# Kernel tuning notes

Measured on AMD Instinct MI355X. Metric: run time of the kernel, lower is better.

Reference implementation:

```python
import jax, jax.numpy as jnp
import numpy as np
from jax import lax


def _causal_depthwise_conv(x, conv_w, conv_b):
    # x: [B, L, D]; conv_w: [D, 1, K]; conv_b: [D]
    K = conv_w.shape[-1]
    xc = jnp.transpose(x, (0, 2, 1))                      # [B, D, L]
    xc = jnp.pad(xc, ((0, 0), (0, 0), (K - 1, 0)))        # left (causal) pad
    D = xc.shape[1]
    y = lax.conv_general_dilated(
        xc, conv_w, window_strides=(1,), padding='VALID',
        dimension_numbers=('NCH', 'OIH', 'NCH'), feature_group_count=D)
    y = y + conv_b[None, :, None]
    return jnp.transpose(y, (0, 2, 1))                    # [B, L, D]


def setup_inputs() -> dict:
    key = jax.random.key(0)
    ks = jax.random.split(key, 7)
    B, L, Dm, S, K = 4, 4096, 2048, 512, 4
    s = 0.02
    x = jax.random.normal(ks[0], (B, L, Dm), dtype=jnp.float32)
    Wxproj = jax.random.normal(ks[1], (2 * S + 1, Dm), dtype=jnp.float32) * s
    Winproj = jax.random.normal(ks[2], (S, Dm), dtype=jnp.float32) * s
    Woutproj = jax.random.normal(ks[3], (Dm, S), dtype=jnp.float32) * s
    conv_w = jax.random.normal(ks[4], (Dm, 1, K), dtype=jnp.float32) * 0.5
    conv_b = jax.random.normal(ks[5], (Dm,), dtype=jnp.float32) * 0.02
    A_log = jnp.log(jnp.arange(1, S + 1, dtype=jnp.float32))
    D = jnp.ones((Dm,), dtype=jnp.float32)
    return {"x": x, "Wxproj": Wxproj, "Winproj": Winproj, "Woutproj": Woutproj,
            "conv_w": conv_w, "conv_b": conv_b, "A_log": A_log, "D": D}


def reference(x, Wxproj, Winproj, Woutproj, conv_w, conv_b, A_log, D):
    S = A_log.shape[0]
    # causal depthwise conv (Conv1d with padding=K-1, truncated to seq_len)
    x_conv = _causal_depthwise_conv(x, conv_w, conv_b)     # [B, L, Dm]
    # SSM parameters from raw x (matches original: x_proj applied to x, not x_conv)
    ssm_params = jnp.einsum('bld,pd->blp', x, Wxproj)      # [B, L, 2S+1]
    Bmat = ssm_params[..., :S]
    Cmat = ssm_params[..., S:2 * S]
    delta = jax.nn.softplus(ssm_params[..., 2 * S:])       # [B, L, 1]
    A = -jnp.exp(A_log)                                    # [S]
    deltaA = jnp.exp(A[None, None, :] * delta)             # [B, L, S]
    x_state = jnp.einsum('bld,sd->bls', x_conv, Winproj)   # [B, L, S]
    Bu = delta * Bmat * x_state                            # [B, L, S]
    # h_t = deltaA_t * h_{t-1} + Bu_t  via associative scan
    def combine(c1, c2):
        a1, b1 = c1
        a2, b2 = c2
        return a1 * a2, a2 * b1 + b2
    _, h = lax.associative_scan(combine, (deltaA, Bu), axis=1)  # [B, L, S]
    h_mod = Cmat * h
    out = jnp.einsum('bls,ds->bld', h_mod, Woutproj) + D[None, None, :] * x_conv
    return out
```

## Files before the change

kernel.cpp:

```cpp
#include <hip/hip_runtime.h>
#include <math.h>

typedef __bf16 bf16_t;
typedef __bf16 bf16x8 __attribute__((ext_vector_type(8)));
typedef __bf16 bf16x4 __attribute__((ext_vector_type(4)));
typedef float  f32x4  __attribute__((ext_vector_type(4)));

constexpr int Bb  = 4;
constexpr int L   = 4096;
constexpr int Dm  = 2048;
constexpr int S   = 512;
constexpr int M   = Bb * L;
constexpr int NP  = 2 * S + 1;
constexpr int NP_PAD = 1280;
constexpr int CL  = 128;
constexpr int NCH = L / CL;
constexpr int TL  = 32;
constexpr int NTC = L / TL;

#define AS1 __attribute__((address_space(1)))
#define AS3 __attribute__((address_space(3)))

__global__ __launch_bounds__(256)
void f2b_kernel(const float* __restrict__ in, bf16_t* __restrict__ out,
                long out8, long in_elems)
{
    long i = (long)blockIdx.x * 256 + threadIdx.x;
    if (i >= out8) return;
    long e = i * 8;
    bf16x8 o;
    if (e + 8 <= in_elems) {
        float4 v0 = *(const float4*)(in + e);
        float4 v1 = *(const float4*)(in + e + 4);
        o[0] = (bf16_t)v0.x; o[1] = (bf16_t)v0.y;
        o[2] = (bf16_t)v0.z; o[3] = (bf16_t)v0.w;
        o[4] = (bf16_t)v1.x; o[5] = (bf16_t)v1.y;
        o[6] = (bf16_t)v1.z; o[7] = (bf16_t)v1.w;
    } else {
        #pragma unroll
        for (int k = 0; k < 8; ++k)
            o[k] = (e + k < in_elems) ? (bf16_t)in[e + k] : (bf16_t)0.f;
    }
    *(bf16x8*)(out + e) = o;
}

__global__ __launch_bounds__(256)
void conv_fused_kernel(const float* __restrict__ x, const float* __restrict__ w,
                       const float* __restrict__ bias,
                       bf16_t* __restrict__ xcb, bf16_t* __restrict__ xb)
{
    const float4* x4 = (const float4*)x;
    int g   = blockIdx.x * 256 + threadIdx.x;
    int d4  = g & 511;
    int rest = g >> 9;
    int c   = rest & (NTC - 1);
    int b   = rest >> 7;
    int d   = d4 * 4;

    float w0[4], w1[4], w2[4], w3[4];
    *(float4*)w0 = *(const float4*)&w[(d + 0) * 4];
    *(float4*)w1 = *(const float4*)&w[(d + 1) * 4];
    *(float4*)w2 = *(const float4*)&w[(d + 2) * 4];
    *(float4*)w3 = *(const float4*)&w[(d + 3) * 4];
    float4 bs = *(const float4*)&bias[d];

    const int l0 = c * TL;
    const size_t rowbase = (size_t)b * L;

    float4 win[3];
    #pragma unroll
    for (int i = 0; i < 3; ++i) {
        int lp = l0 - 3 + i;
        win[i] = (lp >= 0) ? x4[(rowbase + lp) * 512 + d4]
                           : make_float4(0.f, 0.f, 0.f, 0.f);
    }

    #pragma unroll
    for (int t = 0; t < TL; ++t) {
        size_t ri = (rowbase + l0 + t) * 512 + d4;
        float4 cur = x4[ri];
        float4 acc = bs;
        acc.x = fmaf(win[0].x, w0[0], acc.x);
        acc.y = fmaf(win[0].y, w1[0], acc.y);
        acc.z = fmaf(win[0].z, w2[0], acc.z);
        acc.w = fmaf(win[0].w, w3[0], acc.w);
        acc.x = fmaf(win[1].x, w0[1], acc.x);
        acc.y = fmaf(win[1].y, w1[1], acc.y);
        acc.z = fmaf(win[1].z, w2[1], acc.z);
        acc.w = fmaf(win[1].w, w3[1], acc.w);
        acc.x = fmaf(win[2].x, w0[2], acc.x);
        acc.y = fmaf(win[2].y, w1[2], acc.y);
        acc.z = fmaf(win[2].z, w2[2], acc.z);
        acc.w = fmaf(win[2].w, w3[2], acc.w);
        acc.x = fmaf(cur.x, w0[3], acc.x);
        acc.y = fmaf(cur.y, w1[3], acc.y);
        acc.z = fmaf(cur.z, w2[3], acc.z);
        acc.w = fmaf(cur.w, w3[3], acc.w);

        bf16x4 oc, ox;
        oc[0] = (bf16_t)acc.x; oc[1] = (bf16_t)acc.y;
        oc[2] = (bf16_t)acc.z; oc[3] = (bf16_t)acc.w;
        ox[0] = (bf16_t)cur.x; ox[1] = (bf16_t)cur.y;
        ox[2] = (bf16_t)cur.z; ox[3] = (bf16_t)cur.w;
        *(bf16x4*)(xcb + ri * 4) = oc;
        *(bf16x4*)(xb  + ri * 4) = ox;

        win[0] = win[1]; win[1] = win[2]; win[2] = cur;
    }
}

__global__ __launch_bounds__(256)
void delta_kernel(const float* __restrict__ dcol, float* __restrict__ delta)
{
    int i = blockIdx.x * 256 + threadIdx.x;
    if (i < M) {
        float z = dcol[i];
        delta[i] = (z > 20.f) ? z : log1pf(__expf(z));
    }
}

__device__ __forceinline__ void stage_slabA(const bf16_t* __restrict__ A,
    bf16_t* lds, int ldsbase, int row0, int K, int kcol, int mh,
    int wid, int lrow, int cswz)
{
    #pragma unroll
    for (int round = 0; round < 2; ++round) {
        int Rb = round * 128 + mh * 64 + wid * 8;
        const bf16_t* src = A + (size_t)(row0 + Rb + lrow) * K + kcol + cswz;
        __builtin_amdgcn_global_load_lds(
            (AS1 void*)src, (AS3 void*)(lds + ldsbase + Rb * 64), 16, 0, 0);
    }
}

__device__ __forceinline__ void stage_slabB(const bf16_t* __restrict__ B,
    bf16_t* lds, int ldsbase, int col0, int K, int kcol, int nh,
    int wid, int lrow, int cswz)
{
    #pragma unroll
    for (int round = 0; round < 2; ++round) {
        int c  = round * 8 + wid;
        int Rb = (c >> 2) * 64 + nh * 32 + (c & 3) * 8;
        const bf16_t* src = B + (size_t)(col0 + Rb + lrow) * K + kcol + cswz;
        __builtin_amdgcn_global_load_lds(
            (AS1 void*)src, (AS3 void*)(lds + ldsbase + Rb * 64), 16, 0, 0);
    }
}

template <int MH>
__device__ __forceinline__ void load_fragsA(const bf16_t* lds, int Abase,
    int wm, int r, int quad, bf16x8 (&af)[4][2])
{
    #pragma unroll
    for (int i4 = 0; i4 < 4; ++i4) {
        const int R = wm * 128 + (MH * 4 + i4) * 16 + r;
        #pragma unroll
        for (int ks = 0; ks < 2; ++ks)
            af[i4][ks] = *(const bf16x8*)(lds + Abase + R * 64 +
                           ((ks * 32 + quad * 8) ^ ((r & 7) << 3)));
    }
}

template <int NH>
__device__ __forceinline__ void load_fragsB(const bf16_t* lds, int Bbase,
    int wn, int r, int quad, bf16x8 (&bfr)[2][2])
{
    #pragma unroll
    for (int j2 = 0; j2 < 2; ++j2) {
        const int R = wn * 64 + (NH * 2 + j2) * 16 + r;
        #pragma unroll
        for (int ks = 0; ks < 2; ++ks)
            bfr[j2][ks] = *(const bf16x8*)(lds + Bbase + R * 64 +
                            ((ks * 32 + quad * 8) ^ ((r & 7) << 3)));
    }
}

template <int MH, int NH>
__device__ __forceinline__ void do_mfma(bf16x8 (&af)[4][2], bf16x8 (&bfr)[2][2],
                                        f32x4 (&acc)[8][4])
{
    __builtin_amdgcn_s_setprio(1);
    #pragma unroll
    for (int ks = 0; ks < 2; ++ks)
        #pragma unroll
        for (int i4 = 0; i4 < 4; ++i4)
            #pragma unroll
            for (int j2 = 0; j2 < 2; ++j2)
                acc[MH * 4 + i4][NH * 2 + j2] =
                    __builtin_amdgcn_mfma_f32_16x16x32_bf16(
                        af[i4][ks], bfr[j2][ks],
                        acc[MH * 4 + i4][NH * 2 + j2], 0, 0, 0);
    __builtin_amdgcn_s_setprio(0);
}

#define WAITBAR() do { \
    asm volatile("s_waitcnt vmcnt(4)" ::: "memory"); \
    __builtin_amdgcn_s_barrier(); } while (0)

template <int EPI>
__global__ __launch_bounds__(512, 2)
void gemm8p(const bf16_t* __restrict__ A, const bf16_t* __restrict__ B,
            int N, int K, int NT,
            bf16_t* __restrict__ Cb, float* __restrict__ Cf,
            float* __restrict__ dcol,
            const float* __restrict__ e0, const bf16_t* __restrict__ eb)
{
    extern __shared__ __align__(16) char smem_raw[];
    bf16_t* lds = (bf16_t*)smem_raw;

    const int tid  = threadIdx.x;
    const int lane = tid & 63;
    const int wid  = tid >> 6;
    const int wm   = wid >> 2;
    const int wn   = wid & 3;
    const int r    = lane & 15;
    const int quad = lane >> 4;
    const int row0 = blockIdx.x * 256;
    const int col0 = blockIdx.y * 256;
    const int lrow = lane >> 3;
    const int cswz = 8 * ((lane & 7) ^ lrow);

    f32x4 acc[8][4];
    #pragma unroll
    for (int i = 0; i < 8; ++i)
        #pragma unroll
        for (int j = 0; j < 4; ++j) acc[i][j] = (f32x4){0.f, 0.f, 0.f, 0.f};

    stage_slabA(A, lds, 0,     row0, K, 0, 0, wid, lrow, cswz);
    stage_slabB(B, lds, 16384, col0, K, 0, 0, wid, lrow, cswz);
    stage_slabB(B, lds, 16384, col0, K, 0, 1, wid, lrow, cswz);
    stage_slabA(A, lds, 0,     row0, K, 0, 1, wid, lrow, cswz);

    for (int kt = 0; kt < NT; ++kt) {
        const int cur = kt & 1, nxt = cur ^ 1;
        const int Abase = cur * 32768, Bbase = cur * 32768 + 16384;
        const int An = nxt * 32768,   Bn = nxt * 32768 + 16384;
        const int kc = (kt + 1 < NT ? kt + 1 : kt) * 64;

        bf16x8 af[4][2], bfr[2][2];

        WAITBAR();
        load_fragsA<0>(lds, Abase, wm, r, quad, af);
        load_fragsB<0>(lds, Bbase, wn, r, quad, bfr);
        stage_slabA(A, lds, An, row0, K, kc, 0, wid, lrow, cswz);
        do_mfma<0, 0>(af, bfr, acc);

        WAITBAR();
        load_fragsB<1>(lds, Bbase, wn, r, quad, bfr);
        stage_slabB(B, lds, Bn, col0, K, kc, 0, wid, lrow, cswz);
        do_mfma<0, 1>(af, bfr, acc);

        WAITBAR();
        load_fragsA<1>(lds, Abase, wm, r, quad, af);
        stage_slabB(B, lds, Bn, col0, K, kc, 1, wid, lrow, cswz);
        do_mfma<1, 1>(af, bfr, acc);

        load_fragsB<0>(lds, Bbase, wn, r, quad, bfr);
        stage_slabA(A, lds, An, row0, K, kc, 1, wid, lrow, cswz);
        do_mfma<1, 0>(af, bfr, acc);
    }

    #pragma unroll
    for (int i = 0; i < 8; ++i) {
        #pragma unroll
        for (int j = 0; j < 4; ++j) {
            #pragma unroll
            for (int g = 0; g < 4; ++g) {
                int mr = row0 + wm * 128 + i * 16 + quad * 4 + g;
                int nc = col0 + wn * 64 + j * 16 + r;
                float v = acc[i][j][g];
                if (EPI == 0) {
                    if (nc < NP) Cb[(size_t)mr * NP + nc] = (bf16_t)v;
                    if (nc == 2 * S) dcol[mr] = v;
                } else if (EPI == 1) {
                    float Bm = (float)eb[(size_t)mr * NP + nc];
                    Cf[(size_t)mr * N + nc] = e0[mr] * Bm * v;
                } else {
                    float xc = (float)eb[(size_t)mr * N + nc];
                    Cf[(size_t)mr * N + nc] = v + e0[nc] * xc;
                }
            }
        }
    }
}

__global__ __launch_bounds__(256)
void scan_pass1(const float* __restrict__ Bu, const float* __restrict__ delta,
                const float* __restrict__ A_log,
                float* __restrict__ cP, float* __restrict__ cH)
{
    int s = blockIdx.x * 256 + threadIdx.x;
    int c = blockIdx.y;
    int b = blockIdx.z;
    float Acoef = -expf(A_log[s]);
    float P = 1.f, h = 0.f;
    int mbase = b * L + c * CL;
    for (int t = 0; t < CL; ++t) {
        float a = __expf(Acoef * delta[mbase + t]);
        float u = Bu[(size_t)(mbase + t) * S + s];
        h = fmaf(a, h, u);
        P *= a;
    }
    int id = b * S + s;
    cP[(size_t)id * NCH + c] = P;
    cH[(size_t)id * NCH + c] = h;
}

__global__ __launch_bounds__(256)
void scan_pass2(const float* __restrict__ cP, const float* __restrict__ cH,
                float* __restrict__ init)
{
    int id = blockIdx.x * 256 + threadIdx.x;
    if (id < Bb * S) {
        float h = 0.f;
        for (int c = 0; c < NCH; ++c) {
            init[(size_t)id * NCH + c] = h;
            h = fmaf(cP[(size_t)id * NCH + c], h, cH[(size_t)id * NCH + c]);
        }
    }
}

__global__ __launch_bounds__(256)
void scan_pass3(const float* __restrict__ Bu, const float* __restrict__ delta,
                const bf16_t* __restrict__ params_bf,
                const float* __restrict__ A_log,
                const float* __restrict__ init, bf16_t* __restrict__ hmod)
{
    int s = blockIdx.x * 256 + threadIdx.x;
    int c = blockIdx.y;
    int b = blockIdx.z;
    float Acoef = -expf(A_log[s]);
    float h = init[(size_t)(b * S + s) * NCH + c];
    int mbase = b * L + c * CL;
    for (int t = 0; t < CL; ++t) {
        int m = mbase + t;
        float a = __expf(Acoef * delta[m]);
        float u = Bu[(size_t)m * S + s];
        h = fmaf(a, h, u);
        float Cm = (float)params_bf[(size_t)m * NP + S + s];
        hmod[(size_t)m * S + s] = (bf16_t)(Cm * h);
    }
}

extern "C" void kernel_launch(void* const* d_in, const int* in_sizes, int n_in,
                              void* d_out, int out_size, void* d_ws, size_t ws_size,
                              hipStream_t stream)
{
    const float* x        = (const float*)d_in[0];
    const float* Wxproj   = (const float*)d_in[1];
    const float* Winproj  = (const float*)d_in[2];
    const float* Woutproj = (const float*)d_in[3];
    const float* conv_w   = (const float*)d_in[4];
    const float* conv_b   = (const float*)d_in[5];
    const float* A_log    = (const float*)d_in[6];
    const float* Dvec     = (const float*)d_in[7];
    float* out = (float*)d_out;

    float* ws_Bu    = (float*)d_ws;
    float* ws_dcol  = ws_Bu + (size_t)M * S;
    float* ws_delta = ws_dcol + M;
    float* ws_cP    = ws_delta + M;
    float* ws_cH    = ws_cP + (size_t)Bb * S * NCH;
    float* ws_init  = ws_cH + (size_t)Bb * S * NCH;
    bf16_t* params_bf = (bf16_t*)(ws_init + (size_t)Bb * S * NCH);
    bf16_t* x_bf      = params_bf + (size_t)M * NP;
    bf16_t* hmod_bf   = x_bf;
    bf16_t* xconv_bf  = x_bf + (size_t)M * Dm;
    bf16_t* Wx_bf     = xconv_bf + (size_t)M * Dm;
    bf16_t* Win_bf    = Wx_bf + (size_t)NP_PAD * Dm;
    bf16_t* Wout_bf   = Win_bf + (size_t)S * Dm;

    hipFuncSetAttribute((const void*)gemm8p<0>,
                        hipFuncAttributeMaxDynamicSharedMemorySize, 131072);
    hipFuncSetAttribute((const void*)gemm8p<1>,
                        hipFuncAttributeMaxDynamicSharedMemorySize, 131072);
    hipFuncSetAttribute((const void*)gemm8p<2>,
                        hipFuncAttributeMaxDynamicSharedMemorySize, 131072);

    long wx8 = (long)NP_PAD * Dm / 8;
    f2b_kernel<<<(wx8 + 255) / 256, 256, 0, stream>>>(Wxproj, Wx_bf, wx8, (long)NP * Dm);
    long wi8 = (long)S * Dm / 8;
    f2b_kernel<<<(wi8 + 255) / 256, 256, 0, stream>>>(Winproj, Win_bf, wi8, (long)S * Dm);
    f2b_kernel<<<(wi8 + 255) / 256, 256, 0, stream>>>(Woutproj, Wout_bf, wi8, (long)Dm * S);

    conv_fused_kernel<<<(Bb * NTC * 512) / 256, 256, 0, stream>>>(
        x, conv_w, conv_b, xconv_bf, x_bf);

    dim3 g1(M / 256, NP_PAD / 256);
    gemm8p<0><<<g1, 512, 131072, stream>>>(x_bf, Wx_bf, NP, Dm, Dm / 64,
                                           params_bf, nullptr, ws_dcol,
                                           nullptr, nullptr);

    delta_kernel<<<M / 256, 256, 0, stream>>>(ws_dcol, ws_delta);

    dim3 g2(M / 256, S / 256);
    gemm8p<1><<<g2, 512, 131072, stream>>>(xconv_bf, Win_bf, S, Dm, Dm / 64,
                                           nullptr, ws_Bu, nullptr,
                                           ws_delta, params_bf);

    dim3 gs(S / 256, NCH, Bb);
    scan_pass1<<<gs, 256, 0, stream>>>(ws_Bu, ws_delta, A_log, ws_cP, ws_cH);
    scan_pass2<<<(Bb * S) / 256, 256, 0, stream>>>(ws_cP, ws_cH, ws_init);
    scan_pass3<<<gs, 256, 0, stream>>>(ws_Bu, ws_delta, params_bf, A_log,
                                       ws_init, hmod_bf);

    dim3 g3(M / 256, Dm / 256);
    gemm8p<2><<<g3, 512, 131072, stream>>>(hmod_bf, Wout_bf, Dm, S, S / 64,
                                           nullptr, out, nullptr,
                                           Dvec, xconv_bf);
}
```

Measured before the change: 329.7 us.

## Switch GEMMs to 32x32x16 MFMA and split delta column into separate GEMV

All three GEMMs now use 32x32x16 bf16 MFMA tiles instead of 16x16x32, with new LDS fragment loaders and a new epilogue index mapping. This cuts the number of MFMA issues and LDS fragment loads per k-step. The x-projection GEMM now computes only the 1024 B/C columns into a 1024-stride buffer, removing the padded fifth column tile (1280 to 1024). The delta column is computed by a new wave-per-row GEMV kernel that also applies softplus. The cost is an extra pass over x_bf in the GEMV, and the fragment swizzle and epilogue row mapping must match the 32x32 layout exactly to stay correct.

```diff
diff --git a/kernel.cpp b/kernel.cpp
--- a/kernel.cpp
+++ b/kernel.cpp
@@ -5,6 +5,7 @@
 typedef __bf16 bf16x8 __attribute__((ext_vector_type(8)));
 typedef __bf16 bf16x4 __attribute__((ext_vector_type(4)));
 typedef float  f32x4  __attribute__((ext_vector_type(4)));
+typedef float  f32x16 __attribute__((ext_vector_type(16)));
 
 constexpr int Bb  = 4;
 constexpr int L   = 4096;
@@ -12,7 +13,7 @@
 constexpr int S   = 512;
 constexpr int M   = Bb * L;
 constexpr int NP  = 2 * S + 1;
-constexpr int NP_PAD = 1280;
+constexpr int PST = 1024;
 constexpr int CL  = 128;
 constexpr int NCH = L / CL;
 constexpr int TL  = 32;
@@ -110,12 +111,25 @@
 }
 
 __global__ __launch_bounds__(256)
-void delta_kernel(const float* __restrict__ dcol, float* __restrict__ delta)
-{
-    int i = blockIdx.x * 256 + threadIdx.x;
-    if (i < M) {
-        float z = dcol[i];
-        delta[i] = (z > 20.f) ? z : log1pf(__expf(z));
+void gemv_delta(const bf16_t* __restrict__ x_bf, const bf16_t* __restrict__ wdt,
+                float* __restrict__ delta)
+{
+    int m    = blockIdx.x * 4 + (threadIdx.x >> 6);
+    int lane = threadIdx.x & 63;
+    const bf16x8* xr = (const bf16x8*)(x_bf + (size_t)m * Dm);
+    const bf16x8* wr = (const bf16x8*)wdt;
+    float s = 0.f;
+    #pragma unroll
+    for (int i = 0; i < 4; ++i) {
+        bf16x8 a = xr[i * 64 + lane];
+        bf16x8 b = wr[i * 64 + lane];
+        #pragma unroll
+        for (int j = 0; j < 8; ++j) s += (float)a[j] * (float)b[j];
+    }
+    #pragma unroll
+    for (int off = 32; off >= 1; off >>= 1) s += __shfl_xor(s, off, 64);
+    if (lane == 0) {
+        delta[m] = (s > 20.f) ? s : log1pf(__expf(s));
     }
 }
 
@@ -147,48 +161,41 @@
 }
 
 template <int MH>
-__device__ __forceinline__ void load_fragsA(const bf16_t* lds, int Abase,
-    int wm, int r, int quad, bf16x8 (&af)[4][2])
-{
-    #pragma unroll
-    for (int i4 = 0; i4 < 4; ++i4) {
-        const int R = wm * 128 + (MH * 4 + i4) * 16 + r;
-        #pragma unroll
-        for (int ks = 0; ks < 2; ++ks)
-            af[i4][ks] = *(const bf16x8*)(lds + Abase + R * 64 +
-                           ((ks * 32 + quad * 8) ^ ((r & 7) << 3)));
+__device__ __forceinline__ void load_fragsA32(const bf16_t* lds, int Abase,
+    int wm, int l31, int kh, bf16x8 (&af)[2][4])
+{
+    #pragma unroll
+    for (int mi2 = 0; mi2 < 2; ++mi2) {
+        const int R = wm * 128 + (MH * 2 + mi2) * 32 + l31;
+        #pragma unroll
+        for (int ks = 0; ks < 4; ++ks)
+            af[mi2][ks] = *(const bf16x8*)(lds + Abase + R * 64 +
+                            ((ks * 16 + kh * 8) ^ ((R & 7) << 3)));
     }
 }
 
 template <int NH>
-__device__ __forceinline__ void load_fragsB(const bf16_t* lds, int Bbase,
-    int wn, int r, int quad, bf16x8 (&bfr)[2][2])
-{
-    #pragma unroll
-    for (int j2 = 0; j2 < 2; ++j2) {
-        const int R = wn * 64 + (NH * 2 + j2) * 16 + r;
-        #pragma unroll
-        for (int ks = 0; ks < 2; ++ks)
-            bfr[j2][ks] = *(const bf16x8*)(lds + Bbase + R * 64 +
-                            ((ks * 32 + quad * 8) ^ ((r & 7) << 3)));
-    }
+__device__ __forceinline__ void load_fragsB32(const bf16_t* lds, int Bbase,
+    int wn, int l31, int kh, bf16x8 (&bfr)[4])
+{
+    const int R = wn * 64 + NH * 32 + l31;
+    #pragma unroll
+    for (int ks = 0; ks < 4; ++ks)
+        bfr[ks] = *(const bf16x8*)(lds + Bbase + R * 64 +
+                    ((ks * 16 + kh * 8) ^ ((R & 7) << 3)));
 }
 
 template <int MH, int NH>
-__device__ __forceinline__ void do_mfma(bf16x8 (&af)[4][2], bf16x8 (&bfr)[2][2],
-                                        f32x4 (&acc)[8][4])
+__device__ __forceinline__ void do_mfma32(bf16x8 (&af)[2][4], bf16x8 (&bfr)[4],
+                                          f32x16 (&acc)[4][2])
 {
     __builtin_amdgcn_s_setprio(1);
     #pragma unroll
-    for (int ks = 0; ks < 2; ++ks)
-        #pragma unroll
-        for (int i4 = 0; i4 < 4; ++i4)
-            #pragma unroll
-            for (int j2 = 0; j2 < 2; ++j2)
-                acc[MH * 4 + i4][NH * 2 + j2] =
-                    __builtin_amdgcn_mfma_f32_16x16x32_bf16(
-                        af[i4][ks], bfr[j2][ks],
-                        acc[MH * 4 + i4][NH * 2 + j2], 0, 0, 0);
+    for (int ks = 0; ks < 4; ++ks)
+        #pragma unroll
+        for (int mi2 = 0; mi2 < 2; ++mi2)
+            acc[MH * 2 + mi2][NH] = __builtin_amdgcn_mfma_f32_32x32x16_bf16(
+                af[mi2][ks], bfr[ks], acc[MH * 2 + mi2][NH], 0, 0, 0);
     __builtin_amdgcn_s_setprio(0);
 }
 
@@ -201,7 +208,6 @@
 void gemm8p(const bf16_t* __restrict__ A, const bf16_t* __restrict__ B,
             int N, int K, int NT,
             bf16_t* __restrict__ Cb, float* __restrict__ Cf,
-            float* __restrict__ dcol,
             const float* __restrict__ e0, const bf16_t* __restrict__ eb)
 {
     extern __shared__ __align__(16) char smem_raw[];
@@ -212,18 +218,20 @@
     const int wid  = tid >> 6;
     const int wm   = wid >> 2;
     const int wn   = wid & 3;
-    const int r    = lane & 15;
-    const int quad = lane >> 4;
+    const int l31  = lane & 31;
+    const int kh   = lane >> 5;
     const int row0 = blockIdx.x * 256;
     const int col0 = blockIdx.y * 256;
     const int lrow = lane >> 3;
     const int cswz = 8 * ((lane & 7) ^ lrow);
 
-    f32x4 acc[8][4];
-    #pragma unroll
-    for (int i = 0; i < 8; ++i)
-        #pragma unroll
-        for (int j = 0; j < 4; ++j) acc[i][j] = (f32x4){0.f, 0.f, 0.f, 0.f};
+    f32x16 acc[4][2];
+    #pragma unroll
+    for (int i = 0; i < 4; ++i)
+        #pragma unroll
+        for (int j = 0; j < 2; ++j)
+            #pragma unroll
+            for (int g = 0; g < 16; ++g) acc[i][j][g] = 0.f;
 
     stage_slabA(A, lds, 0,     row0, K, 0, 0, wid, lrow, cswz);
     stage_slabB(B, lds, 16384, col0, K, 0, 0, wid, lrow, cswz);
@@ -236,43 +244,42 @@
         const int An = nxt * 32768,   Bn = nxt * 32768 + 16384;
         const int kc = (kt + 1 < NT ? kt + 1 : kt) * 64;
 
-        bf16x8 af[4][2], bfr[2][2];
+        bf16x8 af[2][4], bfr[4];
 
         WAITBAR();
-        load_fragsA<0>(lds, Abase, wm, r, quad, af);
-        load_fragsB<0>(lds, Bbase, wn, r, quad, bfr);
+        load_fragsA32<0>(lds, Abase, wm, l31, kh, af);
+        load_fragsB32<0>(lds, Bbase, wn, l31, kh, bfr);
         stage_slabA(A, lds, An, row0, K, kc, 0, wid, lrow, cswz);
-        do_mfma<0, 0>(af, bfr, acc);
+        do_mfma32<0, 0>(af, bfr, acc);
 
         WAITBAR();
-        load_fragsB<1>(lds, Bbase, wn, r, quad, bfr);
+        load_fragsB32<1>(lds, Bbase, wn, l31, kh, bfr);
         stage_slabB(B, lds, Bn, col0, K, kc, 0, wid, lrow, cswz);
-        do_mfma<0, 1>(af, bfr, acc);
+        do_mfma32<0, 1>(af, bfr, acc);
 
         WAITBAR();
-        load_fragsA<1>(lds, Abase, wm, r, quad, af);
+        load_fragsA32<1>(lds, Abase, wm, l31, kh, af);
         stage_slabB(B, lds, Bn, col0, K, kc, 1, wid, lrow, cswz);
-        do_mfma<1, 1>(af, bfr, acc);
-
-        load_fragsB<0>(lds, Bbase, wn, r, quad, bfr);
+        do_mfma32<1, 1>(af, bfr, acc);
+
+        load_fragsB32<0>(lds, Bbase, wn, l31, kh, bfr);
         stage_slabA(A, lds, An, row0, K, kc, 1, wid, lrow, cswz);
-        do_mfma<1, 0>(af, bfr, acc);
-    }
-
-    #pragma unroll
-    for (int i = 0; i < 8; ++i) {
-        #pragma unroll
-        for (int j = 0; j < 4; ++j) {
+        do_mfma32<1, 0>(af, bfr, acc);
+    }
+
+    #pragma unroll
+    for (int mi = 0; mi < 4; ++mi) {
+        #pragma unroll
+        for (int nj = 0; nj < 2; ++nj) {
             #pragma unroll
-            for (int g = 0; g < 4; ++g) {
-                int mr = row0 + wm * 128 + i * 16 + quad * 4 + g;
-                int nc = col0 + wn * 64 + j * 16 + r;
-                float v = acc[i][j][g];
+            for (int rg = 0; rg < 16; ++rg) {
+                int mr = row0 + wm * 128 + mi * 32 + (rg & 3) + 8 * (rg >> 2) + 4 * kh;
+                int nc = col0 + wn * 64 + nj * 32 + l31;
+                float v = acc[mi][nj][rg];
                 if (EPI == 0) {
-                    if (nc < NP) Cb[(size_t)mr * NP + nc] = (bf16_t)v;
-                    if (nc == 2 * S) dcol[mr] = v;
+                    Cb[(size_t)mr * PST + nc] = (bf16_t)v;
                 } else if (EPI == 1) {
-                    float Bm = (float)eb[(size_t)mr * NP + nc];
+                    float Bm = (float)eb[(size_t)mr * PST + nc];
                     Cf[(size_t)mr * N + nc] = e0[mr] * Bm * v;
                 } else {
                     float xc = (float)eb[(size_t)mr * N + nc];
@@ -336,7 +343,7 @@
         float a = __expf(Acoef * delta[m]);
         float u = Bu[(size_t)m * S + s];
         h = fmaf(a, h, u);
-        float Cm = (float)params_bf[(size_t)m * NP + S + s];
+        float Cm = (float)params_bf[(size_t)m * PST + S + s];
         hmod[(size_t)m * S + s] = (bf16_t)(Cm * h);
     }
 }
@@ -356,17 +363,16 @@
     float* out = (float*)d_out;
 
     float* ws_Bu    = (float*)d_ws;
-    float* ws_dcol  = ws_Bu + (size_t)M * S;
-    float* ws_delta = ws_dcol + M;
+    float* ws_delta = ws_Bu + (size_t)M * S;
     float* ws_cP    = ws_delta + M;
     float* ws_cH    = ws_cP + (size_t)Bb * S * NCH;
     float* ws_init  = ws_cH + (size_t)Bb * S * NCH;
     bf16_t* params_bf = (bf16_t*)(ws_init + (size_t)Bb * S * NCH);
-    bf16_t* x_bf      = params_bf + (size_t)M * NP;
+    bf16_t* x_bf      = params_bf + (size_t)M * PST;
     bf16_t* hmod_bf   = x_bf;
     bf16_t* xconv_bf  = x_bf + (size_t)M * Dm;
     bf16_t* Wx_bf     = xconv_bf + (size_t)M * Dm;
-    bf16_t* Win_bf    = Wx_bf + (size_t)NP_PAD * Dm;
+    bf16_t* Win_bf    = Wx_bf + (size_t)NP * Dm;
     bf16_t* Wout_bf   = Win_bf + (size_t)S * Dm;
 
     hipFuncSetAttribute((const void*)gemm8p<0>,
@@ -376,7 +382,7 @@
     hipFuncSetAttribute((const void*)gemm8p<2>,
                         hipFuncAttributeMaxDynamicSharedMemorySize, 131072);
 
-    long wx8 = (long)NP_PAD * Dm / 8;
+    long wx8 = (long)NP * Dm / 8;
     f2b_kernel<<<(wx8 + 255) / 256, 256, 0, stream>>>(Wxproj, Wx_bf, wx8, (long)NP * Dm);
     long wi8 = (long)S * Dm / 8;
     f2b_kernel<<<(wi8 + 255) / 256, 256, 0, stream>>>(Winproj, Win_bf, wi8, (long)S * Dm);
@@ -385,17 +391,15 @@
     conv_fused_kernel<<<(Bb * NTC * 512) / 256, 256, 0, stream>>>(
         x, conv_w, conv_b, xconv_bf, x_bf);
 
-    dim3 g1(M / 256, NP_PAD / 256);
-    gemm8p<0><<<g1, 512, 131072, stream>>>(x_bf, Wx_bf, NP, Dm, Dm / 64,
-                                           params_bf, nullptr, ws_dcol,
-                                           nullptr, nullptr);
-
-    delta_kernel<<<M / 256, 256, 0, stream>>>(ws_dcol, ws_delta);
+    dim3 g1(M / 256, PST / 256);
+    gemm8p<0><<<g1, 512, 131072, stream>>>(x_bf, Wx_bf, PST, Dm, Dm / 64,
+                                           params_bf, nullptr, nullptr, nullptr);
+
+    gemv_delta<<<M / 4, 256, 0, stream>>>(x_bf, Wx_bf + (size_t)PST * Dm, ws_delta);
 
     dim3 g2(M / 256, S / 256);
     gemm8p<1><<<g2, 512, 131072, stream>>>(xconv_bf, Win_bf, S, Dm, Dm / 64,
-                                           nullptr, ws_Bu, nullptr,
-                                           ws_delta, params_bf);
+                                           nullptr, ws_Bu, ws_delta, params_bf);
 
     dim3 gs(S / 256, NCH, Bb);
     scan_pass1<<<gs, 256, 0, stream>>>(ws_Bu, ws_delta, A_log, ws_cP, ws_cH);
@@ -405,6 +409,5 @@
 
     dim3 g3(M / 256, Dm / 256);
     gemm8p<2><<<g3, 512, 131072, stream>>>(hmod_bf, Wout_bf, Dm, S, S / 64,
-                                           nullptr, out, nullptr,
-                                           Dvec, xconv_bf);
-}
+                                           nullptr, out, Dvec, xconv_bf);
+}
```

Result: faster. 302.8 us (-8.2%).
